# Performance work log

Hardware: AMD Instinct MI355X
Metric: run time of the kernel (lower is better)

The kernel has to match this reference:

```python
import jax, jax.numpy as jnp
import numpy as np

B, T, IN_DIM, D, H, NC = 4, 1024, 231, 512, 8, 1296
NL = 8          # 4 encoders x 2 layers each
DFF = 4 * D     # 2048
DH = D // H
EPS = 1e-5


def _p(k, shape, scale=0.02):
    return jax.random.normal(k, shape, jnp.float32) * scale


def setup_inputs() -> dict:
    key = jax.random.key(0)
    ks = iter(jax.random.split(key, 32))
    z = jnp.zeros
    o = jnp.ones
    return {
        'poses': jax.random.normal(next(ks), (B, T, IN_DIM), jnp.float32),
        'embed_w': _p(next(ks), (D, IN_DIM)), 'embed_b': z((D,)),
        'ln0_g': o((D,)), 'ln0_b': z((D,)),
        'inw': _p(next(ks), (NL, 3 * D, D)), 'inb': z((NL, 3 * D)),
        'outw': _p(next(ks), (NL, D, D)), 'outb': z((NL, D)),
        'ln1g': o((NL, D)), 'ln1b': z((NL, D)),
        'ln2g': o((NL, D)), 'ln2b': z((NL, D)),
        'ff1w': _p(next(ks), (NL, DFF, D)), 'ff1b': z((NL, DFF)),
        'ff2w': _p(next(ks), (NL, D, DFF)), 'ff2b': z((NL, D)),
        'conv1w': _p(next(ks), (D, D, 5)), 'conv1b': z((D,)),
        'bn1g': o((D,)), 'bn1b': z((D,)), 'bn1m': z((D,)), 'bn1v': o((D,)),
        'conv2w': _p(next(ks), (D, D, 3)), 'conv2b': z((D,)),
        'bn2g': o((D,)), 'bn2b': z((D,)), 'bn2m': z((D,)), 'bn2v': o((D,)),
        'fc1w': _p(next(ks), (D // 2, D)), 'fc1b': z((D // 2,)),
        'fc2w': _p(next(ks), (NC, D // 2)), 'fc2b': z((NC,)),
    }


def _ln(x, g, b):
    m = x.mean(-1, keepdims=True)
    v = x.var(-1, keepdims=True)
    return (x - m) / jnp.sqrt(v + EPS) * g + b


def _pos_enc(t_len, d, dtype):
    inv_freq = 1.0 / (10000.0 ** (jnp.arange(0, d, 2, dtype=jnp.float32) / d))
    sin_inp = jnp.arange(t_len, dtype=jnp.float32)[:, None] * inv_freq[None, :]  # [T, d/2]
    # interleave: even idx -> sin, odd idx -> cos
    return jnp.stack([jnp.sin(sin_inp), jnp.cos(sin_inp)], -1).reshape(t_len, d).astype(dtype)


def _layer(x, inw, inb, outw, outb, ln1g, ln1b, ln2g, ln2b, ff1w, ff1b, ff2w, ff2b):
    # pre-norm-style custom layer: norm1 before attention, residual add (no final norm)
    b_, t_, d_ = x.shape
    h = _ln(x, ln1g, ln1b)
    qkv = h @ inw.T + inb
    q, k, v = jnp.split(qkv, 3, axis=-1)
    heads = lambda z: z.reshape(b_, t_, H, DH).transpose(0, 2, 1, 3)  # [B,H,T,dh]
    q, k, v = heads(q), heads(k), heads(v)
    scores = jnp.einsum('bhqd,bhkd->bhqk', q, k) / np.float32(np.sqrt(DH))
    a = jax.nn.softmax(scores, axis=-1)  # explicit weights, as in torch need_weights=True path
    ctx = jnp.einsum('bhqk,bhkd->bhqd', a, v).transpose(0, 2, 1, 3).reshape(b_, t_, d_)
    x = x + ctx @ outw.T + outb
    h2 = _ln(x, ln2g, ln2b)
    ff = jax.nn.relu(h2 @ ff1w.T + ff1b) @ ff2w.T + ff2b
    return x + ff


def _bn(x, g, b, m, v):  # eval-mode BatchNorm1d over [B,C,T]
    return (x - m[None, :, None]) / jnp.sqrt(v + EPS)[None, :, None] * g[None, :, None] + b[None, :, None]


def _conv1d(x, w, b, pad):
    y = jax.lax.conv_general_dilated(x, w, (1,), ((pad, pad),),
                                     dimension_numbers=('NCH', 'OIH', 'NCH'))
    return y + b[None, :, None]


def reference(poses, embed_w, embed_b, ln0_g, ln0_b, inw, inb, outw, outb,
              ln1g, ln1b, ln2g, ln2b, ff1w, ff1b, ff2w, ff2b,
              conv1w, conv1b, bn1g, bn1b, bn1m, bn1v,
              conv2w, conv2b, bn2g, bn2b, bn2m, bn2v,
              fc1w, fc1b, fc2w, fc2b):
    x = _ln(poses @ embed_w.T + embed_b, ln0_g, ln0_b)
    x = x + _pos_enc(x.shape[1], D, x.dtype)[None]

    def block(y, idx):
        for i in idx:
            y = _layer(y, inw[i], inb[i], outw[i], outb[i], ln1g[i], ln1b[i],
                       ln2g[i], ln2b[i], ff1w[i], ff1b[i], ff2w[i], ff2b[i])
        return y

    x = block(x, (0, 1))
    x = block(x, (2, 3)) + x
    x = block(x, (4, 5)) + x
    x = block(x, (6, 7)) + x

    x = x.transpose(0, 2, 1)  # [B, D, T]
    tc = x.shape[-1]
    x = x.reshape(x.shape[0], x.shape[1], tc // 2, 2).mean(-1)  # AvgPool1d(2,2)
    x = jax.nn.gelu(_bn(_conv1d(x, conv1w, conv1b, 2), bn1g, bn1b, bn1m, bn1v), approximate=False)
    x = jax.nn.gelu(_bn(_conv1d(x, conv2w, conv2b, 1), bn2g, bn2b, bn2m, bn2v), approximate=False)
    x = x.transpose(0, 2, 1)  # [B, T/2, D]
    h = jax.nn.gelu(x @ fc1w.T + fc1b, approximate=False)
    return h @ fc2w.T + fc2b  # [B, T/2, num_classes]
```

## Files before the change

kernel.cpp:

```cpp
#include <hip/hip_runtime.h>
#include <math.h>

using u16 = unsigned short;
typedef __attribute__((ext_vector_type(8))) __bf16 bf16x8;
typedef __attribute__((ext_vector_type(4))) float f32x4;

constexpr int Bn = 4, Tn = 1024, INDIM = 231, Dm = 512, NCn = 1296;
constexpr int T2 = 512;
constexpr int Mseq = Bn * Tn;
constexpr int Mtc  = Bn * T2;

enum { EPI_BIAS = 0, EPI_BIAS_RELU, EPI_BIAS_RES, EPI_BIAS_GELU, EPI_SS_GELU };

__device__ __forceinline__ float gelu_exact(float x) {
    return 0.5f * x * (1.0f + erff(x * 0.70710678118654752f));
}
__device__ __forceinline__ u16 f2b(float f) {
    unsigned u = __builtin_bit_cast(unsigned, f);
    return (u16)((u + 0x7FFFu + ((u >> 16) & 1u)) >> 16);
}
__device__ __forceinline__ unsigned pack2(float a, float b) {
    return (unsigned)f2b(a) | ((unsigned)f2b(b) << 16);
}

typedef __attribute__((address_space(3))) void lds_void;
typedef __attribute__((address_space(1))) void g_void;
__device__ __forceinline__ void gld16(const void* g, void* l) {
    __builtin_amdgcn_global_load_lds((g_void*)(uintptr_t)g, (lds_void*)(uintptr_t)l, 16, 0, 0);
}

template<int EPI, bool OB, int IPAD, int OPAD, int MT>
__global__ __launch_bounds__(256)
void gemm_bf(const u16* __restrict__ A, int lda,
             const u16* __restrict__ W,
             float* __restrict__ Cf, u16* __restrict__ Cb,
             int M, int N, int K,
             const float* __restrict__ bias, const float* __restrict__ resid,
             const float* __restrict__ scale, const float* __restrict__ shift)
{
    constexpr int NR = (MT == 128) ? 4 : 2;
    __shared__ __align__(16) u16 As[MT * 32];
    __shared__ __align__(16) u16 Bs[128 * 32];
    const int tid = threadIdx.x;
    const int bm = blockIdx.y * MT, bn = blockIdx.x * 128;
    const int w = tid >> 6, lane = tid & 63;
    const int wr = (MT == 128) ? (w >> 1) * 64 : 0;
    const int wc = (MT == 128) ? (w & 1) * 64 : w * 32;
    const int lr = lane & 15, lhi = lane >> 4;
    const int lkb = lhi * 8;

    const int sr = tid >> 2, sk = (tid & 3) * 8;
    const int r0 = bm + sr;
    const u16* ap0 = A + (size_t)(r0 + 2 * IPAD * (r0 >> 9)) * lda + sk;
    const u16* ap1 = nullptr;
    if constexpr (MT == 128) {
        const int r1 = r0 + 64;
        ap1 = A + (size_t)(r1 + 2 * IPAD * (r1 >> 9)) * lda + sk;
    }
    int wr0 = bn + sr;      if (wr0 >= N) wr0 = N - 1;
    int wr1 = bn + 64 + sr; if (wr1 >= N) wr1 = N - 1;
    const u16* wp0 = W + (size_t)wr0 * K + sk;
    const u16* wp1 = W + (size_t)wr1 * K + sk;
    u16* la0 = &As[tid * 8];
    u16* la1 = (MT == 128) ? &As[2048 + tid * 8] : nullptr;
    u16* lb0 = &Bs[tid * 8];
    u16* lb1 = &Bs[2048 + tid * 8];

    f32x4 acc[4][NR] = {};
    const u16* arp = &As[(wr + lr) * 32 + lkb];
    const u16* brp = &Bs[(wc + lr) * 32 + lkb];

    for (int k0 = 0; k0 < K; k0 += 32) {
        gld16(ap0 + k0, la0);
        if constexpr (MT == 128) gld16(ap1 + k0, la1);
        gld16(wp0 + k0, lb0);
        gld16(wp1 + k0, lb1);
        __syncthreads();
        bf16x8 af[4], bf[NR];
#pragma unroll
        for (int m = 0; m < 4; ++m) af[m] = *(const bf16x8*)(arp + m * 512);
#pragma unroll
        for (int n = 0; n < NR; ++n) bf[n] = *(const bf16x8*)(brp + n * 512);
#pragma unroll
        for (int m = 0; m < 4; ++m)
#pragma unroll
            for (int n = 0; n < NR; ++n)
                acc[m][n] = __builtin_amdgcn_mfma_f32_16x16x32_bf16(af[m], bf[n], acc[m][n], 0, 0, 0);
        __syncthreads();
    }

    const int col0 = bn + wc + lr;
    const int row0 = bm + wr + lhi * 4;
#pragma unroll
    for (int n = 0; n < NR; ++n) {
        const int col = col0 + n * 16;
        if (col >= N) continue;
        float bv = 0.f, sv = 0.f, hv = 0.f;
        if constexpr (EPI == EPI_SS_GELU) { sv = scale[col]; hv = shift[col]; }
        else bv = bias[col];
#pragma unroll
        for (int m = 0; m < 4; ++m) {
#pragma unroll
            for (int j = 0; j < 4; ++j) {
                const int r = row0 + m * 16 + j;
                const int orow = r + OPAD * (2 * (r >> 9) + 1);
                float o = acc[m][n][j];
                if constexpr (EPI == EPI_SS_GELU) {
                    o = gelu_exact(o * sv + hv);
                } else {
                    o += bv;
                    if constexpr (EPI == EPI_BIAS_RELU) o = fmaxf(o, 0.f);
                    if constexpr (EPI == EPI_BIAS_GELU) o = gelu_exact(o);
                    if constexpr (EPI == EPI_BIAS_RES) o += resid[(size_t)r * N + col];
                }
                if constexpr (OB) Cb[(size_t)orow * N + col] = f2b(o);
                else              Cf[(size_t)orow * N + col] = o;
            }
        }
    }
}

__global__ __launch_bounds__(256)
void attn_mfma(const u16* __restrict__ qkv, u16* __restrict__ out)
{
    const int b = blockIdx.z, h = blockIdx.y, q0 = blockIdx.x * 64;
    __shared__ __align__(16) u16 Ks[64 * 64];
    __shared__ __align__(16) u16 Vt[64 * 64];
    __shared__ __align__(16) float Ps[4][16 * 68];
    const int tid = threadIdx.x;
    const int w = tid >> 6, lane = tid & 63;
    const int lr = lane & 15, lhi = lane >> 4;

    bf16x8 qf0, qf1;
    {
        const u16* qp = qkv + (size_t)(b * Tn + q0 + w * 16 + lr) * 1536 + h * 64 + lhi * 8;
        qf0 = *(const bf16x8*)qp;
        qf1 = *(const bf16x8*)(qp + 32);
    }
    float mrow[4], lrow[4];
#pragma unroll
    for (int j = 0; j < 4; ++j) { mrow[j] = -1e30f; lrow[j] = 0.f; }
    f32x4 oacc[4] = {};

    const int kp = tid & 31, dc = (tid >> 5) * 8;

    for (int kt = 0; kt < 16; ++kt) {
        const int kbase = kt * 64;
        __syncthreads();
#pragma unroll
        for (int i = 0; i < 2; ++i) {
            const int row = i * 32 + w * 8 + (lane >> 3);
            const int cg = (lane & 7) ^ (lane >> 3);
            gld16(qkv + (size_t)(b * Tn + kbase + row) * 1536 + 512 + h * 64 + cg * 8,
                  &Ks[(i * 256 + tid) * 8]);
        }
        {
            const u16* v0 = qkv + (size_t)(b * Tn + kbase + 2 * kp) * 1536 + 1024 + h * 64 + dc;
            const uint4 r0v = *(const uint4*)v0;
            const uint4 r1v = *(const uint4*)(v0 + 1536);
            const unsigned a0[4] = {r0v.x, r0v.y, r0v.z, r0v.w};
            const unsigned a1[4] = {r1v.x, r1v.y, r1v.z, r1v.w};
#pragma unroll
            for (int jj = 0; jj < 4; ++jj) {
                const int d0_ = dc + 2 * jj, d1_ = d0_ + 1;
                const unsigned w0 = (a0[jj] & 0xffffu) | (a1[jj] << 16);
                const unsigned w1 = (a0[jj] >> 16) | (a1[jj] & 0xffff0000u);
                *(unsigned*)((char*)Vt + d0_ * 128 + ((4 * kp) ^ ((d0_ & 7) << 4))) = w0;
                *(unsigned*)((char*)Vt + d1_ * 128 + ((4 * kp) ^ ((d1_ & 7) << 4))) = w1;
            }
        }
        __syncthreads();
        f32x4 s[4] = {};
#pragma unroll
        for (int t = 0; t < 4; ++t) {
            const int r = t * 16 + lr;
            const int byt0 = (lhi * 16) ^ ((r & 7) << 4);
            const int byt1 = (64 + lhi * 16) ^ ((r & 7) << 4);
            const bf16x8 k0 = *(const bf16x8*)((const char*)Ks + r * 128 + byt0);
            const bf16x8 k1 = *(const bf16x8*)((const char*)Ks + r * 128 + byt1);
            s[t] = __builtin_amdgcn_mfma_f32_16x16x32_bf16(qf0, k0, s[t], 0, 0, 0);
            s[t] = __builtin_amdgcn_mfma_f32_16x16x32_bf16(qf1, k1, s[t], 0, 0, 0);
        }
        float sv[4][4];
#pragma unroll
        for (int t = 0; t < 4; ++t)
#pragma unroll
            for (int j = 0; j < 4; ++j) sv[t][j] = s[t][j] * 0.125f;
        float f[4];
#pragma unroll
        for (int j = 0; j < 4; ++j) {
            float mt = fmaxf(fmaxf(sv[0][j], sv[1][j]), fmaxf(sv[2][j], sv[3][j]));
            mt = fmaxf(mt, __shfl_xor(mt, 1));
            mt = fmaxf(mt, __shfl_xor(mt, 2));
            mt = fmaxf(mt, __shfl_xor(mt, 4));
            mt = fmaxf(mt, __shfl_xor(mt, 8));
            const float mnew = fmaxf(mrow[j], mt);
            f[j] = __expf(mrow[j] - mnew);
            mrow[j] = mnew;
            float sum = 0.f;
#pragma unroll
            for (int t = 0; t < 4; ++t) {
                sv[t][j] = __expf(sv[t][j] - mnew);
                sum += sv[t][j];
            }
            sum += __shfl_xor(sum, 1);
            sum += __shfl_xor(sum, 2);
            sum += __shfl_xor(sum, 4);
            sum += __shfl_xor(sum, 8);
            lrow[j] = lrow[j] * f[j] + sum;
        }
#pragma unroll
        for (int t = 0; t < 4; ++t)
#pragma unroll
            for (int j = 0; j < 4; ++j) oacc[t][j] *= f[j];
#pragma unroll
        for (int t = 0; t < 4; ++t)
#pragma unroll
            for (int j = 0; j < 4; ++j)
                Ps[w][(lhi * 4 + j) * 68 + t * 16 + lr] = sv[t][j];
        __syncthreads();
        bf16x8 pf[2];
#pragma unroll
        for (int s2 = 0; s2 < 2; ++s2) {
            const float* pr = &Ps[w][lr * 68 + s2 * 32 + lhi * 8];
            const float4 pa = *(const float4*)pr;
            const float4 pb = *(const float4*)(pr + 4);
            uint4 pk;
            pk.x = pack2(pa.x, pa.y); pk.y = pack2(pa.z, pa.w);
            pk.z = pack2(pb.x, pb.y); pk.w = pack2(pb.z, pb.w);
            pf[s2] = __builtin_bit_cast(bf16x8, pk);
        }
#pragma unroll
        for (int t = 0; t < 4; ++t) {
            const int rd = t * 16 + lr;
            const int byt0 = (lhi * 16) ^ ((rd & 7) << 4);
            const int byt1 = (64 + lhi * 16) ^ ((rd & 7) << 4);
            const bf16x8 v0f = *(const bf16x8*)((const char*)Vt + rd * 128 + byt0);
            const bf16x8 v1f = *(const bf16x8*)((const char*)Vt + rd * 128 + byt1);
            oacc[t] = __builtin_amdgcn_mfma_f32_16x16x32_bf16(pf[0], v0f, oacc[t], 0, 0, 0);
            oacc[t] = __builtin_amdgcn_mfma_f32_16x16x32_bf16(pf[1], v1f, oacc[t], 0, 0, 0);
        }
    }
#pragma unroll
    for (int j = 0; j < 4; ++j) {
        const float inv = 1.f / lrow[j];
        const size_t grow = (size_t)(b * Tn + q0 + w * 16 + lhi * 4 + j) * 512 + h * 64;
#pragma unroll
        for (int t = 0; t < 4; ++t)
            out[grow + t * 16 + lr] = f2b(oacc[t][j] * inv);
    }
}

__device__ __forceinline__ float pe_val(int t, int d) {
    const int k = d & ~1;
    const float invf = __expf(-(float)k * (9.210340371976184f / 512.f));
    const float ang = (float)t * invf;
    return (d & 1) ? cosf(ang) : sinf(ang);
}

template<bool OB, bool PE>
__global__ __launch_bounds__(256)
void ln_k(const float* __restrict__ in, float* __restrict__ outf, u16* __restrict__ outb,
          const float* __restrict__ g, const float* __restrict__ bsh)
{
    const int lane = threadIdx.x & 63;
    const int row = blockIdx.x * 4 + (threadIdx.x >> 6);
    const float* src = in + (size_t)row * Dm;
    const int c0 = lane * 4;
    const float4 v0 = *(const float4*)(src + c0);
    const float4 v1 = *(const float4*)(src + 256 + c0);
    float s  = v0.x + v0.y + v0.z + v0.w + v1.x + v1.y + v1.z + v1.w;
    float ss = v0.x * v0.x + v0.y * v0.y + v0.z * v0.z + v0.w * v0.w
             + v1.x * v1.x + v1.y * v1.y + v1.z * v1.z + v1.w * v1.w;
#pragma unroll
    for (int off = 32; off; off >>= 1) { s += __shfl_xor(s, off); ss += __shfl_xor(ss, off); }
    const float mean = s * (1.f / 512.f);
    const float var = ss * (1.f / 512.f) - mean * mean;
    const float rstd = rsqrtf(var + 1e-5f);
    const float4 g0 = *(const float4*)(g + c0),   g1 = *(const float4*)(g + 256 + c0);
    const float4 b0 = *(const float4*)(bsh + c0), b1 = *(const float4*)(bsh + 256 + c0);
    float o0[4] = {(v0.x - mean) * rstd * g0.x + b0.x, (v0.y - mean) * rstd * g0.y + b0.y,
                   (v0.z - mean) * rstd * g0.z + b0.z, (v0.w - mean) * rstd * g0.w + b0.w};
    float o1[4] = {(v1.x - mean) * rstd * g1.x + b1.x, (v1.y - mean) * rstd * g1.y + b1.y,
                   (v1.z - mean) * rstd * g1.z + b1.z, (v1.w - mean) * rstd * g1.w + b1.w};
    if constexpr (PE) {
        const int t = row & (Tn - 1);
#pragma unroll
        for (int j = 0; j < 4; ++j) { o0[j] += pe_val(t, c0 + j); o1[j] += pe_val(t, 256 + c0 + j); }
    }
    if constexpr (OB) {
        *(ushort4*)(outb + (size_t)row * Dm + c0) =
            make_ushort4(f2b(o0[0]), f2b(o0[1]), f2b(o0[2]), f2b(o0[3]));
        *(ushort4*)(outb + (size_t)row * Dm + 256 + c0) =
            make_ushort4(f2b(o1[0]), f2b(o1[1]), f2b(o1[2]), f2b(o1[3]));
    } else {
        *(float4*)(outf + (size_t)row * Dm + c0) = make_float4(o0[0], o0[1], o0[2], o0[3]);
        *(float4*)(outf + (size_t)row * Dm + 256 + c0) = make_float4(o1[0], o1[1], o1[2], o1[3]);
    }
}

__global__ void copy_k(const float* __restrict__ a, float* __restrict__ o, int n4) {
    const int i = blockIdx.x * blockDim.x + threadIdx.x;
    if (i < n4) ((float4*)o)[i] = ((const float4*)a)[i];
}
__global__ void add_k(float* __restrict__ o, const float* __restrict__ a, int n4) {
    const int i = blockIdx.x * blockDim.x + threadIdx.x;
    if (i < n4) {
        float4 x = ((float4*)o)[i];
        const float4 y = ((const float4*)a)[i];
        x.x += y.x; x.y += y.y; x.z += y.z; x.w += y.w;
        ((float4*)o)[i] = x;
    }
}
__global__ void cvt_layer_k(const float* __restrict__ inw, const float* __restrict__ outw,
                            const float* __restrict__ ff1w, const float* __restrict__ ff2w,
                            int layer, u16* __restrict__ dst) {
    const int i = (blockIdx.x * 256 + threadIdx.x) * 8;
    const float* src;
    if (i < 786432)       src = inw  + (size_t)layer *  786432 + i;
    else if (i < 1048576) src = outw + (size_t)layer *  262144 + (i - 786432);
    else if (i < 2097152) src = ff1w + (size_t)layer * 1048576 + (i - 1048576);
    else                  src = ff2w + (size_t)layer * 1048576 + (i - 2097152);
    const float4 a = *(const float4*)src, b = *(const float4*)(src + 4);
    uint4 o; o.x = pack2(a.x, a.y); o.y = pack2(a.z, a.w); o.z = pack2(b.x, b.y); o.w = pack2(b.z, b.w);
    *(uint4*)(dst + i) = o;
}
__global__ void cvt8_k(const float* __restrict__ in, u16* __restrict__ out, int n8) {
    const int t = blockIdx.x * 256 + threadIdx.x;
    if (t >= n8) return;
    const int i = t * 8;
    const float4 a = *(const float4*)(in + i), b = *(const float4*)(in + i + 4);
    uint4 o; o.x = pack2(a.x, a.y); o.y = pack2(a.z, a.w); o.z = pack2(b.x, b.y); o.w = pack2(b.z, b.w);
    *(uint4*)(out + i) = o;
}
__global__ void padposes_k(const float* __restrict__ p, u16* __restrict__ o, int rows) {
    const int i = blockIdx.x * 256 + threadIdx.x;
    if (i >= rows * 256) return;
    const int r = i >> 8, c = i & 255;
    o[i] = (c < INDIM) ? f2b(p[r * INDIM + c]) : (u16)0;
}
__global__ void zero_k(uint4* __restrict__ p, int n16) {
    const int i = blockIdx.x * 256 + threadIdx.x;
    if (i < n16) p[i] = make_uint4(0, 0, 0, 0);
}
__global__ void pool_k(const float* __restrict__ x, u16* __restrict__ o) {
    const int i = blockIdx.x * 256 + threadIdx.x;
    if (i >= 262144) return;
    const int flat = i * 4;
    const int row = flat >> 9, col = flat & 511;
    const int b = row >> 9, t2 = row & 511;
    const float* p0 = x + ((size_t)(b * Tn + 2 * t2) << 9) + col;
    const float4 u = *(const float4*)p0;
    const float4 w = *(const float4*)(p0 + 512);
    ushort4 r = make_ushort4(f2b(0.5f * (u.x + w.x)), f2b(0.5f * (u.y + w.y)),
                             f2b(0.5f * (u.z + w.z)), f2b(0.5f * (u.w + w.w)));
    *(ushort4*)(o + (((size_t)(b * 516 + 2 + t2)) << 9) + col) = r;
}
__global__ void wtrans_k(const float* __restrict__ w, u16* __restrict__ wt, int KS) {
    const int i = blockIdx.x * 256 + threadIdx.x;
    if (i >= 512 * 512 * KS) return;
    const int o = i / (512 * KS);
    const int rem = i - o * (512 * KS);
    const int c = rem / KS, ks = rem - c * KS;
    wt[((size_t)o * KS + ks) * 512 + c] = f2b(w[i]);
}
__global__ void bnfold_k(const float* __restrict__ g, const float* __restrict__ b,
                         const float* __restrict__ m, const float* __restrict__ v,
                         const float* __restrict__ cb, float* __restrict__ sc, float* __restrict__ sh) {
    const int i = blockIdx.x * blockDim.x + threadIdx.x;
    if (i < Dm) {
        const float s = g[i] * rsqrtf(v[i] + 1e-5f);
        sc[i] = s;
        sh[i] = (cb[i] - m[i]) * s + b[i];
    }
}

extern "C" void kernel_launch(void* const* d_in, const int* in_sizes, int n_in,
                              void* d_out, int out_size, void* d_ws, size_t ws_size,
                              hipStream_t stream)
{
    (void)in_sizes; (void)n_in; (void)out_size; (void)ws_size;
    const float* poses   = (const float*)d_in[0];
    const float* embed_w = (const float*)d_in[1];
    const float* embed_b = (const float*)d_in[2];
    const float* ln0_g   = (const float*)d_in[3];
    const float* ln0_b   = (const float*)d_in[4];
    const float* inw  = (const float*)d_in[5];
    const float* inb  = (const float*)d_in[6];
    const float* outw = (const float*)d_in[7];
    const float* outb = (const float*)d_in[8];
    const float* ln1g = (const float*)d_in[9];
    const float* ln1b = (const float*)d_in[10];
    const float* ln2g = (const float*)d_in[11];
    const float* ln2b = (const float*)d_in[12];
    const float* ff1w = (const float*)d_in[13];
    const float* ff1b = (const float*)d_in[14];
    const float* ff2w = (const float*)d_in[15];
    const float* ff2b = (const float*)d_in[16];
    const float* conv1w = (const float*)d_in[17];
    const float* conv1b = (const float*)d_in[18];
    const float* bn1g = (const float*)d_in[19];
    const float* bn1b = (const float*)d_in[20];
    const float* bn1m = (const float*)d_in[21];
    const float* bn1v = (const float*)d_in[22];
    const float* conv2w = (const float*)d_in[23];
    const float* conv2b = (const float*)d_in[24];
    const float* bn2g = (const float*)d_in[25];
    const float* bn2b = (const float*)d_in[26];
    const float* bn2m = (const float*)d_in[27];
    const float* bn2v = (const float*)d_in[28];
    const float* fc1w = (const float*)d_in[29];
    const float* fc1b = (const float*)d_in[30];
    const float* fc2w = (const float*)d_in[31];
    const float* fc2b = (const float*)d_in[32];

    char* ws = (char*)d_ws;
    float* x    = (float*)(ws);
    float* resb = (float*)(ws + (8u << 20));
    char* big   = ws + (16u << 20);
    u16* qkv16  = (u16*)big;
    u16* hb16   = (u16*)(ws + (40u << 20));
    u16* ctx16  = (u16*)(ws + (44u << 20));
    u16* ff116  = (u16*)(ws + (48u << 20));
    u16* wbuf   = (u16*)(ws + (64u << 20));
    float* outp = (float*)d_out;

    char* tb = big;
    u16* poolpad = (u16*)tb;
    u16* c1pad   = (u16*)(tb + 2113536);
    u16* c2o16   = (u16*)(tb + 4218880);
    u16* f1o16   = (u16*)(tb + 6316032);
    u16* w1t16   = (u16*)(tb + 7364608);
    u16* w2t16   = (u16*)(tb + 9986048);
    u16* fc1w16  = (u16*)(tb + 11558912);
    u16* fc2w16  = (u16*)(tb + 11821056);
    float* sc1   = (float*)(tb + 12484608);
    float* sh1   = sc1 + 512;
    float* sc2   = sh1 + 512;
    float* sh2   = sc2 + 512;
    u16* embw16  = (u16*)(tb + (20u << 20));
    float* embout = (float*)(tb + (16u << 20));
    u16* pospad  = hb16;

    const u16* wq  = wbuf;
    const u16* wo  = wbuf + 786432;
    const u16* wf1 = wbuf + 1048576;
    const u16* wf2 = wbuf + 2097152;

    padposes_k<<<4096, 256, 0, stream>>>(poses, pospad, 4096);
    padposes_k<<<512, 256, 0, stream>>>(embed_w, embw16, 512);
    gemm_bf<EPI_BIAS, false, 0, 0, 64><<<dim3(4, 64), 256, 0, stream>>>(
        pospad, 256, embw16, embout, nullptr, Mseq, 512, 256, embed_b, nullptr, nullptr, nullptr);
    ln_k<false, true><<<1024, 256, 0, stream>>>(embout, x, nullptr, ln0_g, ln0_b);

    for (int i = 0; i < 8; ++i) {
        if (i == 2 || i == 4 || i == 6)
            copy_k<<<2048, 256, 0, stream>>>(x, resb, 1 << 19);
        cvt_layer_k<<<1536, 256, 0, stream>>>(inw, outw, ff1w, ff2w, i, wbuf);
        ln_k<true, false><<<1024, 256, 0, stream>>>(x, nullptr, hb16, ln1g + i * 512, ln1b + i * 512);
        gemm_bf<EPI_BIAS, true, 0, 0, 128><<<dim3(12, 32), 256, 0, stream>>>(
            hb16, 512, wq, nullptr, qkv16, Mseq, 1536, 512, inb + i * 1536, nullptr, nullptr, nullptr);
        attn_mfma<<<dim3(16, 8, 4), 256, 0, stream>>>(qkv16, ctx16);
        gemm_bf<EPI_BIAS_RES, false, 0, 0, 64><<<dim3(4, 64), 256, 0, stream>>>(
            ctx16, 512, wo, x, nullptr, Mseq, 512, 512, outb + i * 512, x, nullptr, nullptr);
        ln_k<true, false><<<1024, 256, 0, stream>>>(x, nullptr, hb16, ln2g + i * 512, ln2b + i * 512);
        gemm_bf<EPI_BIAS_RELU, true, 0, 0, 128><<<dim3(16, 32), 256, 0, stream>>>(
            hb16, 512, wf1, nullptr, ff116, Mseq, 2048, 512, ff1b + i * 2048, nullptr, nullptr, nullptr);
        gemm_bf<EPI_BIAS_RES, false, 0, 0, 64><<<dim3(4, 64), 256, 0, stream>>>(
            ff116, 2048, wf2, x, nullptr, Mseq, 512, 2048, ff2b + i * 512, x, nullptr, nullptr);
        if (i == 3 || i == 5 || i == 7)
            add_k<<<2048, 256, 0, stream>>>(x, resb, 1 << 19);
    }

    zero_k<<<516, 256, 0, stream>>>((uint4*)poolpad, 132096);
    pool_k<<<1024, 256, 0, stream>>>(x, poolpad);
    wtrans_k<<<5120, 256, 0, stream>>>(conv1w, w1t16, 5);
    bnfold_k<<<2, 256, 0, stream>>>(bn1g, bn1b, bn1m, bn1v, conv1b, sc1, sh1);
    zero_k<<<514, 256, 0, stream>>>((uint4*)c1pad, 131584);
    gemm_bf<EPI_SS_GELU, true, 2, 1, 64><<<dim3(4, 32), 256, 0, stream>>>(
        poolpad, 512, w1t16, nullptr, c1pad, Mtc, 512, 2560, nullptr, nullptr, sc1, sh1);
    wtrans_k<<<3072, 256, 0, stream>>>(conv2w, w2t16, 3);
    bnfold_k<<<2, 256, 0, stream>>>(bn2g, bn2b, bn2m, bn2v, conv2b, sc2, sh2);
    gemm_bf<EPI_SS_GELU, true, 1, 0, 64><<<dim3(4, 32), 256, 0, stream>>>(
        c1pad, 512, w2t16, nullptr, c2o16, Mtc, 512, 1536, nullptr, nullptr, sc2, sh2);
    cvt8_k<<<64, 256, 0, stream>>>(fc1w, fc1w16, 16384);
    cvt8_k<<<162, 256, 0, stream>>>(fc2w, fc2w16, 41472);
    gemm_bf<EPI_BIAS_GELU, true, 0, 0, 64><<<dim3(2, 32), 256, 0, stream>>>(
        c2o16, 512, fc1w16, nullptr, f1o16, Mtc, 256, 512, fc1b, nullptr, nullptr, nullptr);
    gemm_bf<EPI_BIAS, false, 0, 0, 64><<<dim3(11, 32), 256, 0, stream>>>(
        f1o16, 256, fc2w16, outp, nullptr, Mtc, 1296, 256, fc2b, nullptr, nullptr, nullptr);
}
```

Before: 1.495 ms.

## Double-buffer GEMM and attention LDS tiles with BK=64 and swizzled layout

The GEMM now stages 64-wide K tiles into two swizzled LDS buffers and prefetches the next tile while computing the current one, so each iteration needs one barrier instead of two. The attention kernel likewise double-buffers K and V^T, issuing next-tile loads before the QK^T MFMAs. It also replaces the block barrier around the per-wave P buffer with an LDS waitcnt, folds the 1/sqrt(d) scale into exp2, and sets wave priority around the MFMA sections. This doubles LDS use, which may lower occupancy, and relies on Ps being private to each wave.

New measurement: 1.304 ms. -12.7%, faster.

```diff
diff --git a/kernel.cpp b/kernel.cpp
--- a/kernel.cpp
+++ b/kernel.cpp
@@ -39,54 +39,69 @@
              const float* __restrict__ scale, const float* __restrict__ shift)
 {
     constexpr int NR = (MT == 128) ? 4 : 2;
-    __shared__ __align__(16) u16 As[MT * 32];
-    __shared__ __align__(16) u16 Bs[128 * 32];
+    constexpr int AI = MT / 32;
+    __shared__ __align__(16) u16 As[2][MT * 64];
+    __shared__ __align__(16) u16 Bs[2][128 * 64];
     const int tid = threadIdx.x;
     const int bm = blockIdx.y * MT, bn = blockIdx.x * 128;
     const int w = tid >> 6, lane = tid & 63;
     const int wr = (MT == 128) ? (w >> 1) * 64 : 0;
     const int wc = (MT == 128) ? (w & 1) * 64 : w * 32;
     const int lr = lane & 15, lhi = lane >> 4;
-    const int lkb = lhi * 8;
-
-    const int sr = tid >> 2, sk = (tid & 3) * 8;
-    const int r0 = bm + sr;
-    const u16* ap0 = A + (size_t)(r0 + 2 * IPAD * (r0 >> 9)) * lda + sk;
-    const u16* ap1 = nullptr;
-    if constexpr (MT == 128) {
-        const int r1 = r0 + 64;
-        ap1 = A + (size_t)(r1 + 2 * IPAD * (r1 >> 9)) * lda + sk;
-    }
-    int wr0 = bn + sr;      if (wr0 >= N) wr0 = N - 1;
-    int wr1 = bn + 64 + sr; if (wr1 >= N) wr1 = N - 1;
-    const u16* wp0 = W + (size_t)wr0 * K + sk;
-    const u16* wp1 = W + (size_t)wr1 * K + sk;
-    u16* la0 = &As[tid * 8];
-    u16* la1 = (MT == 128) ? &As[2048 + tid * 8] : nullptr;
-    u16* lb0 = &Bs[tid * 8];
-    u16* lb1 = &Bs[2048 + tid * 8];
+
+    const int srow = tid >> 3;
+    const int cg8 = ((tid & 7) ^ (srow & 7)) * 8;
+    const u16* apg[AI];
+#pragma unroll
+    for (int i = 0; i < AI; ++i) {
+        const int r = bm + i * 32 + srow;
+        apg[i] = A + (size_t)(r + 2 * IPAD * (r >> 9)) * lda + cg8;
+    }
+    const u16* wpg[4];
+#pragma unroll
+    for (int i = 0; i < 4; ++i) {
+        int r = bn + i * 32 + srow; if (r >= N) r = N - 1;
+        wpg[i] = W + (size_t)r * K + cg8;
+    }
 
     f32x4 acc[4][NR] = {};
-    const u16* arp = &As[(wr + lr) * 32 + lkb];
-    const u16* brp = &Bs[(wc + lr) * 32 + lkb];
-
-    for (int k0 = 0; k0 < K; k0 += 32) {
-        gld16(ap0 + k0, la0);
-        if constexpr (MT == 128) gld16(ap1 + k0, la1);
-        gld16(wp0 + k0, lb0);
-        gld16(wp1 + k0, lb1);
-        __syncthreads();
-        bf16x8 af[4], bf[NR];
-#pragma unroll
-        for (int m = 0; m < 4; ++m) af[m] = *(const bf16x8*)(arp + m * 512);
-#pragma unroll
-        for (int n = 0; n < NR; ++n) bf[n] = *(const bf16x8*)(brp + n * 512);
-#pragma unroll
-        for (int m = 0; m < 4; ++m)
-#pragma unroll
-            for (int n = 0; n < NR; ++n)
-                acc[m][n] = __builtin_amdgcn_mfma_f32_16x16x32_bf16(af[m], bf[n], acc[m][n], 0, 0, 0);
-        __syncthreads();
+    const int nt = K >> 6;
+
+#pragma unroll
+    for (int i = 0; i < AI; ++i) gld16(apg[i], &As[0][(i * 256 + tid) * 8]);
+#pragma unroll
+    for (int i = 0; i < 4; ++i)  gld16(wpg[i], &Bs[0][(i * 256 + tid) * 8]);
+    __syncthreads();
+
+    for (int t = 0; t < nt; ++t) {
+        const int cur = t & 1;
+        if (t + 1 < nt) {
+            const int k0 = (t + 1) * 64;
+#pragma unroll
+            for (int i = 0; i < AI; ++i) gld16(apg[i] + k0, &As[cur ^ 1][(i * 256 + tid) * 8]);
+#pragma unroll
+            for (int i = 0; i < 4; ++i)  gld16(wpg[i] + k0, &Bs[cur ^ 1][(i * 256 + tid) * 8]);
+        }
+#pragma unroll
+        for (int ks = 0; ks < 2; ++ks) {
+            bf16x8 af[4], bfv[NR];
+#pragma unroll
+            for (int m = 0; m < 4; ++m) {
+                const int R = wr + lr + m * 16;
+                af[m] = *(const bf16x8*)((const char*)&As[cur][0] + R * 128 + (((ks * 4 + lhi) ^ (R & 7)) * 16));
+            }
+#pragma unroll
+            for (int n = 0; n < NR; ++n) {
+                const int R = wc + lr + n * 16;
+                bfv[n] = *(const bf16x8*)((const char*)&Bs[cur][0] + R * 128 + (((ks * 4 + lhi) ^ (R & 7)) * 16));
+            }
+#pragma unroll
+            for (int m = 0; m < 4; ++m)
+#pragma unroll
+                for (int n = 0; n < NR; ++n)
+                    acc[m][n] = __builtin_amdgcn_mfma_f32_16x16x32_bf16(af[m], bfv[n], acc[m][n], 0, 0, 0);
+        }
+        if (t + 1 < nt) __syncthreads();
     }
 
     const int col0 = bn + wc + lr;
@@ -124,12 +139,15 @@
 void attn_mfma(const u16* __restrict__ qkv, u16* __restrict__ out)
 {
     const int b = blockIdx.z, h = blockIdx.y, q0 = blockIdx.x * 64;
-    __shared__ __align__(16) u16 Ks[64 * 64];
-    __shared__ __align__(16) u16 Vt[64 * 64];
+    __shared__ __align__(16) u16 Ks[2][64 * 64];
+    __shared__ __align__(16) u16 Vt[2][64 * 64];
     __shared__ __align__(16) float Ps[4][16 * 68];
     const int tid = threadIdx.x;
     const int w = tid >> 6, lane = tid & 63;
     const int lr = lane & 15, lhi = lane >> 4;
+    const int kp = tid & 31, dc = (tid >> 5) * 8;
+    const int krow = w * 8 + (lane >> 3);
+    const int kcg = (((lane & 7) ^ (lane >> 3))) * 8;
 
     bf16x8 qf0, qf1;
     {
@@ -142,66 +160,74 @@
     for (int j = 0; j < 4; ++j) { mrow[j] = -1e30f; lrow[j] = 0.f; }
     f32x4 oacc[4] = {};
 
-    const int kp = tid & 31, dc = (tid >> 5) * 8;
+    auto stageK = [&](int kb, int bsel) {
+#pragma unroll
+        for (int i = 0; i < 2; ++i)
+            gld16(qkv + (size_t)(b * Tn + kb + i * 32 + krow) * 1536 + 512 + h * 64 + kcg,
+                  &Ks[bsel][(i * 256 + tid) * 8]);
+    };
+    auto loadV = [&](int kb, uint4& rA, uint4& rB) {
+        const u16* vp = qkv + (size_t)(b * Tn + kb + 2 * kp) * 1536 + 1024 + h * 64 + dc;
+        rA = *(const uint4*)vp;
+        rB = *(const uint4*)(vp + 1536);
+    };
+    auto vtrans = [&](uint4 rA, uint4 rB, int bsel) {
+        const unsigned a0[4] = {rA.x, rA.y, rA.z, rA.w};
+        const unsigned a1[4] = {rB.x, rB.y, rB.z, rB.w};
+#pragma unroll
+        for (int jj = 0; jj < 4; ++jj) {
+            const int d0_ = dc + 2 * jj, d1_ = d0_ + 1;
+            const unsigned w0 = (a0[jj] & 0xffffu) | (a1[jj] << 16);
+            const unsigned w1 = (a0[jj] >> 16) | (a1[jj] & 0xffff0000u);
+            *(unsigned*)((char*)&Vt[bsel][0] + d0_ * 128 + ((4 * kp) ^ ((d0_ & 7) << 4))) = w0;
+            *(unsigned*)((char*)&Vt[bsel][0] + d1_ * 128 + ((4 * kp) ^ ((d1_ & 7) << 4))) = w1;
+        }
+    };
+
+    uint4 vA, vB;
+    stageK(0, 0);
+    loadV(0, vA, vB);
+    vtrans(vA, vB, 0);
+    __syncthreads();
+
+    constexpr float C1 = 0.125f * 1.44269504f;
 
     for (int kt = 0; kt < 16; ++kt) {
-        const int kbase = kt * 64;
-        __syncthreads();
-#pragma unroll
-        for (int i = 0; i < 2; ++i) {
-            const int row = i * 32 + w * 8 + (lane >> 3);
-            const int cg = (lane & 7) ^ (lane >> 3);
-            gld16(qkv + (size_t)(b * Tn + kbase + row) * 1536 + 512 + h * 64 + cg * 8,
-                  &Ks[(i * 256 + tid) * 8]);
-        }
-        {
-            const u16* v0 = qkv + (size_t)(b * Tn + kbase + 2 * kp) * 1536 + 1024 + h * 64 + dc;
-            const uint4 r0v = *(const uint4*)v0;
-            const uint4 r1v = *(const uint4*)(v0 + 1536);
-            const unsigned a0[4] = {r0v.x, r0v.y, r0v.z, r0v.w};
-            const unsigned a1[4] = {r1v.x, r1v.y, r1v.z, r1v.w};
-#pragma unroll
-            for (int jj = 0; jj < 4; ++jj) {
-                const int d0_ = dc + 2 * jj, d1_ = d0_ + 1;
-                const unsigned w0 = (a0[jj] & 0xffffu) | (a1[jj] << 16);
-                const unsigned w1 = (a0[jj] >> 16) | (a1[jj] & 0xffff0000u);
-                *(unsigned*)((char*)Vt + d0_ * 128 + ((4 * kp) ^ ((d0_ & 7) << 4))) = w0;
-                *(unsigned*)((char*)Vt + d1_ * 128 + ((4 * kp) ^ ((d1_ & 7) << 4))) = w1;
-            }
-        }
-        __syncthreads();
+        const int cur = kt & 1;
+        const bool more = kt < 15;
+        if (more) {
+            stageK((kt + 1) * 64, cur ^ 1);
+            loadV((kt + 1) * 64, vA, vB);
+        }
+        __builtin_amdgcn_s_setprio(1);
         f32x4 s[4] = {};
 #pragma unroll
         for (int t = 0; t < 4; ++t) {
             const int r = t * 16 + lr;
-            const int byt0 = (lhi * 16) ^ ((r & 7) << 4);
-            const int byt1 = (64 + lhi * 16) ^ ((r & 7) << 4);
-            const bf16x8 k0 = *(const bf16x8*)((const char*)Ks + r * 128 + byt0);
-            const bf16x8 k1 = *(const bf16x8*)((const char*)Ks + r * 128 + byt1);
+            const bf16x8 k0 = *(const bf16x8*)((const char*)&Ks[cur][0] + r * 128 + ((lhi * 16) ^ ((r & 7) << 4)));
+            const bf16x8 k1 = *(const bf16x8*)((const char*)&Ks[cur][0] + r * 128 + ((64 + lhi * 16) ^ ((r & 7) << 4)));
             s[t] = __builtin_amdgcn_mfma_f32_16x16x32_bf16(qf0, k0, s[t], 0, 0, 0);
             s[t] = __builtin_amdgcn_mfma_f32_16x16x32_bf16(qf1, k1, s[t], 0, 0, 0);
         }
-        float sv[4][4];
-#pragma unroll
-        for (int t = 0; t < 4; ++t)
-#pragma unroll
-            for (int j = 0; j < 4; ++j) sv[t][j] = s[t][j] * 0.125f;
+        __builtin_amdgcn_s_setprio(0);
         float f[4];
 #pragma unroll
         for (int j = 0; j < 4; ++j) {
-            float mt = fmaxf(fmaxf(sv[0][j], sv[1][j]), fmaxf(sv[2][j], sv[3][j]));
+            float mt = fmaxf(fmaxf(s[0][j], s[1][j]), fmaxf(s[2][j], s[3][j]));
             mt = fmaxf(mt, __shfl_xor(mt, 1));
             mt = fmaxf(mt, __shfl_xor(mt, 2));
             mt = fmaxf(mt, __shfl_xor(mt, 4));
             mt = fmaxf(mt, __shfl_xor(mt, 8));
             const float mnew = fmaxf(mrow[j], mt);
-            f[j] = __expf(mrow[j] - mnew);
+            f[j] = exp2f((mrow[j] - mnew) * C1);
             mrow[j] = mnew;
+            const float nb = mnew * C1;
             float sum = 0.f;
 #pragma unroll
             for (int t = 0; t < 4; ++t) {
-                sv[t][j] = __expf(sv[t][j] - mnew);
-                sum += sv[t][j];
+                const float p = exp2f(fmaf(s[t][j], C1, -nb));
+                Ps[w][(lhi * 4 + j) * 68 + t * 16 + lr] = p;
+                sum += p;
             }
             sum += __shfl_xor(sum, 1);
             sum += __shfl_xor(sum, 2);
@@ -213,12 +239,7 @@
         for (int t = 0; t < 4; ++t)
 #pragma unroll
             for (int j = 0; j < 4; ++j) oacc[t][j] *= f[j];
-#pragma unroll
-        for (int t = 0; t < 4; ++t)
-#pragma unroll
-            for (int j = 0; j < 4; ++j)
-                Ps[w][(lhi * 4 + j) * 68 + t * 16 + lr] = sv[t][j];
-        __syncthreads();
+        asm volatile("s_waitcnt lgkmcnt(0)" ::: "memory");
         bf16x8 pf[2];
 #pragma unroll
         for (int s2 = 0; s2 < 2; ++s2) {
@@ -230,15 +251,19 @@
             pk.z = pack2(pb.x, pb.y); pk.w = pack2(pb.z, pb.w);
             pf[s2] = __builtin_bit_cast(bf16x8, pk);
         }
+        __builtin_amdgcn_s_setprio(1);
 #pragma unroll
         for (int t = 0; t < 4; ++t) {
             const int rd = t * 16 + lr;
-            const int byt0 = (lhi * 16) ^ ((rd & 7) << 4);
-            const int byt1 = (64 + lhi * 16) ^ ((rd & 7) << 4);
-            const bf16x8 v0f = *(const bf16x8*)((const char*)Vt + rd * 128 + byt0);
-            const bf16x8 v1f = *(const bf16x8*)((const char*)Vt + rd * 128 + byt1);
+            const bf16x8 v0f = *(const bf16x8*)((const char*)&Vt[cur][0] + rd * 128 + ((lhi * 16) ^ ((rd & 7) << 4)));
+            const bf16x8 v1f = *(const bf16x8*)((const char*)&Vt[cur][0] + rd * 128 + ((64 + lhi * 16) ^ ((rd & 7) << 4)));
             oacc[t] = __builtin_amdgcn_mfma_f32_16x16x32_bf16(pf[0], v0f, oacc[t], 0, 0, 0);
             oacc[t] = __builtin_amdgcn_mfma_f32_16x16x32_bf16(pf[1], v1f, oacc[t], 0, 0, 0);
+        }
+        __builtin_amdgcn_s_setprio(0);
+        if (more) {
+            vtrans(vA, vB, cur ^ 1);
+            __syncthreads();
         }
     }
 #pragma unroll
```
